# Performance work log

Measured on AMD Instinct MI355X. Metric: run time of the kernel, lower is better.

## Reference

```python
import jax, jax.numpy as jnp
import numpy as np

IMG = 800.0
STRIDES = (4, 8, 16, 32)
SIZES = (32.0, 64.0, 128.0, 256.0)
RATIOS = (0.5, 1.0, 2.0)
A = 3
PRE_NMS_K = 1000
POST_NMS = 512
NMS_TH = 0.7
POOL = 7
_MEAN = np.array([0.485, 0.456, 0.406], np.float32).reshape(3, 1, 1)
_STD = np.array([0.229, 0.224, 0.225], np.float32).reshape(3, 1, 1)


def _conv(x, w, stride=1):
    # x: [C,H,W], w: [O,I,kh,kw]
    return jax.lax.conv_general_dilated(x[None], w, (stride, stride), 'SAME',
                                        dimension_numbers=('NCHW', 'OIHW', 'NCHW'))[0]


def _make_anchors(fh, fw, stride, size):
    cy = (np.arange(fh, dtype=np.float32) + 0.5) * stride
    cx = (np.arange(fw, dtype=np.float32) + 0.5) * stride
    ws = np.array([size / np.sqrt(r) for r in RATIOS], np.float32)
    hs = np.array([size * np.sqrt(r) for r in RATIOS], np.float32)
    gy, gx = np.meshgrid(cy, cx, indexing='ij')
    x1 = gx[..., None] - ws / 2; y1 = gy[..., None] - hs / 2
    x2 = gx[..., None] + ws / 2; y2 = gy[..., None] + hs / 2
    return jnp.asarray(np.stack([x1, y1, x2, y2], -1).reshape(-1, 4))  # [fh*fw*A,4]


def _decode(anchors, deltas):
    aw = anchors[:, 2] - anchors[:, 0]; ah = anchors[:, 3] - anchors[:, 1]
    acx = anchors[:, 0] + aw * 0.5; acy = anchors[:, 1] + ah * 0.5
    dw = jnp.clip(deltas[:, 2], -4.0, 4.0); dh = jnp.clip(deltas[:, 3], -4.0, 4.0)
    cx = acx + deltas[:, 0] * aw; cy = acy + deltas[:, 1] * ah
    w = aw * jnp.exp(dw); h = ah * jnp.exp(dh)
    boxes = jnp.stack([cx - w * 0.5, cy - h * 0.5, cx + w * 0.5, cy + h * 0.5], -1)
    return jnp.clip(boxes, 0.0, IMG)


def _nms(boxes, scores, iou_th, max_out):
    # Greedy NMS with fixed output size (jit-compatible).
    x1, y1, x2, y2 = boxes[:, 0], boxes[:, 1], boxes[:, 2], boxes[:, 3]
    areas = (x2 - x1) * (y2 - y1)

    def body(i, state):
        s, keep = state
        idx = jnp.argmax(s)
        keep = keep.at[i].set(idx)
        ix1 = jnp.maximum(x1, x1[idx]); iy1 = jnp.maximum(y1, y1[idx])
        ix2 = jnp.minimum(x2, x2[idx]); iy2 = jnp.minimum(y2, y2[idx])
        inter = jnp.maximum(ix2 - ix1, 0.0) * jnp.maximum(iy2 - iy1, 0.0)
        iou = inter / (areas + areas[idx] - inter + 1e-6)
        return jnp.where(iou > iou_th, -jnp.inf, s), keep

    _, keep = jax.lax.fori_loop(0, max_out, body, (scores, jnp.zeros(max_out, jnp.int32)))
    return keep


def _roi_align(feat, rois, scale):
    # feat: [C,H,W]; rois: [N,4] in image coords; bilinear, 1 sample per bin.
    C, H, W = feat.shape
    n = rois.shape[0]
    x1 = rois[:, 0] * scale; y1 = rois[:, 1] * scale
    bw = (rois[:, 2] - rois[:, 0]) * scale / POOL
    bh = (rois[:, 3] - rois[:, 1]) * scale / POOL
    j = jnp.arange(POOL, dtype=feat.dtype) + 0.5
    gx = jnp.broadcast_to((x1[:, None] + j * bw[:, None] - 0.5)[:, None, :], (n, POOL, POOL))
    gy = jnp.broadcast_to((y1[:, None] + j * bh[:, None] - 0.5)[:, :, None], (n, POOL, POOL))
    fx = jnp.clip(jnp.floor(gx), 0.0, W - 1); fy = jnp.clip(jnp.floor(gy), 0.0, H - 1)
    x0 = fx.astype(jnp.int32); y0 = fy.astype(jnp.int32)
    x1i = jnp.minimum(x0 + 1, W - 1); y1i = jnp.minimum(y0 + 1, H - 1)
    wx = jnp.clip(gx - fx, 0.0, 1.0); wy = jnp.clip(gy - fy, 0.0, 1.0)
    v = (feat[:, y0, x0] * (1 - wy) * (1 - wx) + feat[:, y0, x1i] * (1 - wy) * wx
         + feat[:, y1i, x0] * wy * (1 - wx) + feat[:, y1i, x1i] * wy * wx)  # [C,N,P,P]
    return jnp.transpose(v, (1, 0, 2, 3))  # [N,C,P,P]


def _forward(x, stem_w, c2_w, c3_w, c4_w, c5_w, fpn2_w, fpn3_w, fpn4_w, fpn5_w,
             rpn_w, rpn_cls_w, rpn_box_w, fc1_w, fc1_b, fc2_w, fc2_b,
             cls_w, cls_b, breg_w, breg_b):
    x = (x - _MEAN) / _STD  # ImageNet normalize
    h = jax.nn.relu(_conv(x, stem_w, 2))      # [64,400,400]
    c2 = jax.nn.relu(_conv(h, c2_w, 2))       # [256,200,200] stride 4
    c3 = jax.nn.relu(_conv(c2, c3_w, 2))      # stride 8
    c4 = jax.nn.relu(_conv(c3, c4_w, 2))      # stride 16
    c5 = jax.nn.relu(_conv(c4, c5_w, 2))      # stride 32
    feats = [_conv(c2, fpn2_w), _conv(c3, fpn3_w), _conv(c4, fpn4_w), _conv(c5, fpn5_w)]

    boxes_l, scores_l = [], []
    for lvl, f in enumerate(feats):
        t = jax.nn.relu(_conv(f, rpn_w))
        fh, fw = f.shape[1], f.shape[2]
        logits = jnp.transpose(_conv(t, rpn_cls_w), (1, 2, 0)).reshape(-1)  # [fh*fw*A]
        deltas = jnp.transpose(_conv(t, rpn_box_w).reshape(A, 4, fh, fw), (2, 3, 0, 1)).reshape(-1, 4)
        anchors = _make_anchors(fh, fw, STRIDES[lvl], SIZES[lvl])
        dec = _decode(anchors, deltas)
        k = min(PRE_NMS_K, logits.shape[0])
        sc, idx = jax.lax.top_k(logits, k)
        boxes_l.append(dec[idx]); scores_l.append(sc)

    boxes = jnp.concatenate(boxes_l, 0)
    scores = jnp.concatenate(scores_l, 0)
    keep = _nms(boxes, scores, NMS_TH, POST_NMS)
    props = boxes[keep]  # [POST_NMS,4]

    pooled = _roi_align(feats[0], props, 1.0 / STRIDES[0])  # [N,256,7,7]
    v = pooled.reshape(POST_NMS, -1)
    v = jax.nn.relu(v @ fc1_w + fc1_b)
    v = jax.nn.relu(v @ fc2_w + fc2_b)
    return v @ cls_w + cls_b, v @ breg_w + breg_b, props, scores[keep]


def setup_inputs() -> dict:
    key = jax.random.key(0)
    ks = jax.random.split(key, 18)

    def he(k, shape):
        fan_in = int(np.prod(shape[1:])) if len(shape) == 4 else shape[0]
        return jax.random.normal(k, shape, jnp.float32) * float(np.sqrt(2.0 / fan_in))

    inp = {'x': jax.random.uniform(ks[0], (3, 800, 800), jnp.float32)}
    inp['stem_w'] = he(ks[1], (64, 3, 7, 7))
    inp['c2_w'] = he(ks[2], (256, 64, 3, 3))
    for i, name in enumerate(['c3_w', 'c4_w', 'c5_w', 'fpn2_w', 'fpn3_w', 'fpn4_w', 'fpn5_w', 'rpn_w']):
        inp[name] = he(ks[3 + i], (256, 256, 3, 3))
    inp['rpn_cls_w'] = he(ks[11], (3, 256, 1, 1))
    inp['rpn_box_w'] = he(ks[12], (12, 256, 1, 1))
    inp['fc1_w'] = he(ks[13], (12544, 1024)); inp['fc1_b'] = jnp.zeros((1024,), jnp.float32)
    inp['fc2_w'] = he(ks[14], (1024, 1024)); inp['fc2_b'] = jnp.zeros((1024,), jnp.float32)
    inp['cls_w'] = he(ks[15], (1024, 2)); inp['cls_b'] = jnp.zeros((2,), jnp.float32)
    inp['breg_w'] = he(ks[16], (1024, 8)); inp['breg_b'] = jnp.zeros((8,), jnp.float32)
    return inp


def reference(x, stem_w, c2_w, c3_w, c4_w, c5_w, fpn2_w, fpn3_w, fpn4_w, fpn5_w,
              rpn_w, rpn_cls_w, rpn_box_w, fc1_w, fc1_b, fc2_w, fc2_b,
              cls_w, cls_b, breg_w, breg_b):
    return _forward(x, stem_w, c2_w, c3_w, c4_w, c5_w, fpn2_w, fpn3_w, fpn4_w, fpn5_w,
                    rpn_w, rpn_cls_w, rpn_box_w, fc1_w, fc1_b, fc2_w, fc2_b,
                    cls_w, cls_b, breg_w, breg_b)
```

## Files before the change

kernel.cpp:

```cpp
#include <hip/hip_runtime.h>
#include <math.h>


#define DI __device__ __forceinline__

typedef short short8 __attribute__((ext_vector_type(8)));
typedef float float16v __attribute__((ext_vector_type(16)));

DI unsigned fkey(float f) {
  unsigned u = __float_as_uint(f);
  return (u & 0x80000000u) ? ~u : (u | 0x80000000u);
}

DI unsigned short f2bf(float f) {
  unsigned u = __float_as_uint(f);
  unsigned r = (u + 0x7FFFu + ((u >> 16) & 1u)) >> 16;
  return (unsigned short)r;
}

DI void rp256(const float* src, float* dst, int j) {
  int co = j & 15; int r = j >> 4; int kk = r % 9; int r2 = r / 9;
  int ci = r2 & 255; int z = r2 >> 8;
  dst[j] = src[((size_t)(z * 16 + co) * 256 + ci) * 9 + kk];
}

__global__ void repack_all(
    const float* __restrict__ wf2, const float* __restrict__ wf3,
    const float* __restrict__ wrpn, const float* __restrict__ wc2,
    const float* __restrict__ wc3, const float* __restrict__ wc4,
    const float* __restrict__ wc5, const float* __restrict__ wf4,
    const float* __restrict__ wf5, const float* __restrict__ wstem,
    float* __restrict__ wpkA, float* __restrict__ wpkB,
    float* __restrict__ wpkC, float* __restrict__ wpkD,
    float* __restrict__ wpkE, float* __restrict__ wpkF,
    float* __restrict__ wpkG, float* __restrict__ wpkH,
    float* __restrict__ wpkI, float* __restrict__ wpkS) {
  const int SZ = 589824, SZD = 147456;
  const int D0 = 3 * SZ;
  const int D1 = D0 + SZD;
  const int D2 = D1 + 5 * SZ;
  const int D3 = D2 + 9408;
  int i = blockIdx.x * 256 + threadIdx.x;
  if (i >= D3) return;
  if (i < D0) {
    const float* src = (i < SZ) ? wf2 : (i < 2 * SZ) ? wf3 : wrpn;
    float* dst = (i < SZ) ? wpkA : (i < 2 * SZ) ? wpkB : wpkC;
    rp256(src, dst, i % SZ);
  } else if (i < D1) {
    int j = i - D0;
    int co = j & 15; int r = j >> 4; int kk = r % 9; int r2 = r / 9;
    int ci = r2 & 63; int z = r2 >> 6;
    wpkD[j] = wc2[((size_t)(z * 16 + co) * 64 + ci) * 9 + kk];
  } else if (i < D2) {
    int j = i - D1;
    int seg = j / SZ; j -= seg * SZ;
    const float* src = (seg == 0) ? wc3 : (seg == 1) ? wc4
                       : (seg == 2) ? wc5 : (seg == 3) ? wf4 : wf5;
    float* dst = (seg == 0) ? wpkE : (seg == 1) ? wpkF
                 : (seg == 2) ? wpkG : (seg == 3) ? wpkH : wpkI;
    rp256(src, dst, j);
  } else {
    int j = i - D2;
    int co = j & 3; int r = j >> 2;
    int k = r % 147; int z = r / 147;
    wpkS[j] = wstem[(size_t)(z * 4 + co) * 147 + k];
  }
}

__global__ __launch_bounds__(256) void stem_conv(const float* __restrict__ x,
                                                 const float* __restrict__ wpkS,
                                                 float* __restrict__ out) {
  __shared__ float tin[3 * 37 * 37];
  const int x0 = blockIdx.x * 16, y0 = blockIdx.y * 16, co0 = blockIdx.z * 4;
  const int tid = threadIdx.x;
  const int ix0 = x0 * 2 - 2, iy0 = y0 * 2 - 2;
  const float mean[3] = {0.485f, 0.456f, 0.406f};
  const float stdv[3] = {0.229f, 0.224f, 0.225f};
  for (int i = tid; i < 3 * 37 * 37; i += 256) {
    int c = i / 1369, r = i % 1369, yy = r / 37, xx = r % 37;
    int gy = iy0 + yy, gx = ix0 + xx;
    float v = 0.f;
    if ((unsigned)gy < 800u && (unsigned)gx < 800u)
      v = __fdiv_rn(__fsub_rn(x[c * 640000 + gy * 800 + gx], mean[c]), stdv[c]);
    tin[i] = v;
  }
  __syncthreads();
  const int tx = tid & 15, ty = tid >> 4;
  float acc[4] = {0.f, 0.f, 0.f, 0.f};
  const float4* wq = (const float4*)(wpkS + (size_t)blockIdx.z * 588);
  for (int c = 0; c < 3; ++c)
    for (int ky = 0; ky < 7; ++ky)
#pragma unroll
      for (int kx = 0; kx < 7; ++kx) {
        float v = tin[c * 1369 + (ty * 2 + ky) * 37 + (tx * 2 + kx)];
        float4 wv = wq[c * 49 + ky * 7 + kx];
        acc[0] = fmaf(v, wv.x, acc[0]);
        acc[1] = fmaf(v, wv.y, acc[1]);
        acc[2] = fmaf(v, wv.z, acc[2]);
        acc[3] = fmaf(v, wv.w, acc[3]);
      }
  int ox = x0 + tx, oy = y0 + ty;
#pragma unroll
  for (int co = 0; co < 4; ++co)
    out[(size_t)(co0 + co) * 160000 + oy * 400 + ox] = fmaxf(acc[co], 0.f);
}

template <int CHUNK, bool RELU, bool TT>
DI void conv32_body(const float* __restrict__ in,
                    const float* __restrict__ wpk, float* __restrict__ out,
                    int Cin, int Hin, int Win, int Hout, int Wout, int bx,
                    int by, int bz,
                    float (*tin2)[((CHUNK * 612 + 255) / 256) * 256]) {
  constexpr int TILE = CHUNK * 612;
  constexpr int NS = (TILE + 255) / 256;
  const int tid = threadIdx.x;
  const int tx = tid & 15, ty = tid >> 4;
  const int x0 = bx * 32, y0 = by * 16;
  const int ix0 = x0 - 1, iy0 = y0 - 1;
  const size_t HWin = (size_t)Hin * Win;

  int goff[NS];
#pragma unroll
  for (int j = 0; j < NS; ++j) {
    int e = j * 256 + tid;
    int c = e / 612, r = e % 612;
    int yy = r / 34, xx = r % 34;
    int gy = iy0 + yy, gx = ix0 + xx;
    bool ok = (e < TILE) && ((unsigned)gy < (unsigned)Hin) &&
              ((unsigned)gx < (unsigned)Win);
    goff[j] = ok ? (int)((size_t)c * HWin + (size_t)gy * Win + gx) : -1;
  }

  float acc0[16], acc1[16];
#pragma unroll
  for (int co = 0; co < 16; ++co) { acc0[co] = 0.f; acc1[co] = 0.f; }

  float stg[NS];
#pragma unroll
  for (int j = 0; j < NS; ++j)
    stg[j] = (goff[j] >= 0) ? in[goff[j]] : 0.f;
#pragma unroll
  for (int j = 0; j < NS; ++j) tin2[0][j * 256 + tid] = stg[j];
  __syncthreads();

  int buf = 0;
  for (int cb = 0; cb < Cin; cb += CHUNK) {
    const bool more = (cb + CHUNK) < Cin;
    if (more) {
      const float* gsrc = in + (size_t)(cb + CHUNK) * HWin;
#pragma unroll
      for (int j = 0; j < NS; ++j)
        stg[j] = (goff[j] >= 0) ? gsrc[goff[j]] : 0.f;
    }
    for (int ci = 0; ci < CHUNK; ++ci) {
      const float4* wq = (const float4*)(wpk +
          ((size_t)bz * Cin + (size_t)(cb + ci)) * 144);
#pragma unroll
      for (int ky = 0; ky < 3; ++ky) {
        const float* tb = &tin2[buf][ci * 612 + (ty + ky) * 34 + 2 * tx];
        float2 d0 = *(const float2*)tb;
        float2 d1 = *(const float2*)(tb + 2);
#pragma unroll
        for (int kx = 0; kx < 3; ++kx) {
          float v0 = (kx == 0) ? d0.x : (kx == 1) ? d0.y : d1.x;
          float v1 = (kx == 0) ? d0.y : (kx == 1) ? d1.x : d1.y;
          const int kk = ky * 3 + kx;
          float4 w0 = wq[kk * 4 + 0];
          float4 w1 = wq[kk * 4 + 1];
          float4 w2 = wq[kk * 4 + 2];
          float4 w3 = wq[kk * 4 + 3];
          acc0[0]  = fmaf(v0, w0.x, acc0[0]);
          acc0[1]  = fmaf(v0, w0.y, acc0[1]);
          acc0[2]  = fmaf(v0, w0.z, acc0[2]);
          acc0[3]  = fmaf(v0, w0.w, acc0[3]);
          acc1[0]  = fmaf(v1, w0.x, acc1[0]);
          acc1[1]  = fmaf(v1, w0.y, acc1[1]);
          acc1[2]  = fmaf(v1, w0.z, acc1[2]);
          acc1[3]  = fmaf(v1, w0.w, acc1[3]);
          acc0[4]  = fmaf(v0, w1.x, acc0[4]);
          acc0[5]  = fmaf(v0, w1.y, acc0[5]);
          acc0[6]  = fmaf(v0, w1.z, acc0[6]);
          acc0[7]  = fmaf(v0, w1.w, acc0[7]);
          acc1[4]  = fmaf(v1, w1.x, acc1[4]);
          acc1[5]  = fmaf(v1, w1.y, acc1[5]);
          acc1[6]  = fmaf(v1, w1.z, acc1[6]);
          acc1[7]  = fmaf(v1, w1.w, acc1[7]);
          acc0[8]  = fmaf(v0, w2.x, acc0[8]);
          acc0[9]  = fmaf(v0, w2.y, acc0[9]);
          acc0[10] = fmaf(v0, w2.z, acc0[10]);
          acc0[11] = fmaf(v0, w2.w, acc0[11]);
          acc1[8]  = fmaf(v1, w2.x, acc1[8]);
          acc1[9]  = fmaf(v1, w2.y, acc1[9]);
          acc1[10] = fmaf(v1, w2.z, acc1[10]);
          acc1[11] = fmaf(v1, w2.w, acc1[11]);
          acc0[12] = fmaf(v0, w3.x, acc0[12]);
          acc0[13] = fmaf(v0, w3.y, acc0[13]);
          acc0[14] = fmaf(v0, w3.z, acc0[14]);
          acc0[15] = fmaf(v0, w3.w, acc0[15]);
          acc1[12] = fmaf(v1, w3.x, acc1[12]);
          acc1[13] = fmaf(v1, w3.y, acc1[13]);
          acc1[14] = fmaf(v1, w3.z, acc1[14]);
          acc1[15] = fmaf(v1, w3.w, acc1[15]);
        }
      }
    }
    if (more) {
#pragma unroll
      for (int j = 0; j < NS; ++j) tin2[buf ^ 1][j * 256 + tid] = stg[j];
    }
    __syncthreads();
    buf ^= 1;
  }

  const int co0 = bz * 16;
  int oy = y0 + ty;
  if (oy < Hout) {
    int ox = x0 + 2 * tx;
    if (TT) {
      if (ox < Wout) {
        float* o = out + (size_t)(oy * Wout + ox) * 256 + co0;
#pragma unroll
        for (int co = 0; co < 16; ++co) {
          float a = acc0[co];
          if (RELU) a = fmaxf(a, 0.f);
          o[co] = a;
        }
      }
      if (ox + 1 < Wout) {
        float* o = out + (size_t)(oy * Wout + ox + 1) * 256 + co0;
#pragma unroll
        for (int co = 0; co < 16; ++co) {
          float a = acc1[co];
          if (RELU) a = fmaxf(a, 0.f);
          o[co] = a;
        }
      }
    } else {
      if (ox + 1 < Wout) {
#pragma unroll
        for (int co = 0; co < 16; ++co) {
          float a = acc0[co], b = acc1[co];
          if (RELU) { a = fmaxf(a, 0.f); b = fmaxf(b, 0.f); }
          float2 st; st.x = a; st.y = b;
          *(float2*)&out[(size_t)(co0 + co) * Hout * Wout +
                         (size_t)oy * Wout + ox] = st;
        }
      } else if (ox < Wout) {
#pragma unroll
        for (int co = 0; co < 16; ++co) {
          float a = acc0[co];
          if (RELU) a = fmaxf(a, 0.f);
          out[(size_t)(co0 + co) * Hout * Wout + (size_t)oy * Wout + ox] = a;
        }
      }
    }
  }
// ... 310 lines not shown
    float dh = fminf(fmaxf(a[3 + an * 4 + 3], -4.f), 4.f);
    float cx = __fadd_rn(acx, __fmul_rn(dx, aw));
    float cy = __fadd_rn(acy, __fmul_rn(dy, ah));
    float w_ = __fmul_rn(aw, expf(dw));
    float h_ = __fmul_rn(ah, expf(dh));
    int idx = p * 3 + an;
    float* bo = boxes4 + boff;
    bo[idx * 4 + 0] =
        fminf(fmaxf(__fsub_rn(cx, __fmul_rn(w_, 0.5f)), 0.f), 800.f);
    bo[idx * 4 + 1] =
        fminf(fmaxf(__fsub_rn(cy, __fmul_rn(h_, 0.5f)), 0.f), 800.f);
    bo[idx * 4 + 2] =
        fminf(fmaxf(__fadd_rn(cx, __fmul_rn(w_, 0.5f)), 0.f), 800.f);
    bo[idx * 4 + 3] =
        fminf(fmaxf(__fadd_rn(cy, __fmul_rn(h_, 0.5f)), 0.f), 800.f);
    scores4[soff + idx] = a[an];
    atomicAdd(&hist4[lvl * 65536 + (fkey(a[an]) >> 16)], 1);
  }
}

__global__ __launch_bounds__(256) void scan_hi_all(int* __restrict__ hist4,
                                                   int* __restrict__ sel4) {
  __shared__ int csum[256];
  int* hist = hist4 + blockIdx.x * 65536;
  int* sel = sel4 + blockIdx.x * 8;
  const int k = 1000;
  int t = threadIdx.x;
  int s = 0;
  for (int i = 0; i < 256; ++i) s += hist[t * 256 + i];
  csum[t] = s;
  __syncthreads();
  if (t == 0) {
    int cum = 0;
    bool done = false;
    for (int c = 255; c >= 0; --c) {
      if (cum + csum[c] >= k) {
        int cc = cum;
        for (int b = c * 256 + 255;; --b) {
          int h = hist[b];
          if (cc + h >= k) {
            sel[0] = b; sel[1] = k - cc; sel[2] = cc;
            done = true;
            break;
          }
          cc += h;
        }
        break;
      }
      cum += csum[c];
    }
    if (!done) { sel[0] = 0; sel[1] = k - cum; sel[2] = cum; }
  }
  __syncthreads();
  int4 z4; z4.x = 0; z4.y = 0; z4.z = 0; z4.w = 0;
  for (int i = t; i < 16384; i += 256) ((int4*)hist)[i] = z4;
}

DI void lvl_seg(int b, int& lvl, int& base, int& N, int& soff, int& boff) {
  if (b < 469) { lvl = 0; base = 0; N = 120000; soff = 0; boff = 0; }
  else if (b < 587) { lvl = 1; base = 469; N = 30000; soff = 120000;
                      boff = 480000; }
  else if (b < 617) { lvl = 2; base = 587; N = 7500; soff = 150000;
                      boff = 600000; }
  else { lvl = 3; base = 617; N = 1875; soff = 157500; boff = 630000; }
}

__global__ void hist_lo_all(const float* __restrict__ scores4,
                            const int* __restrict__ sel4,
                            int* __restrict__ hist4) {
  int lvl, base, N, soff, boff;
  lvl_seg(blockIdx.x, lvl, base, N, soff, boff);
  int i = (blockIdx.x - base) * 256 + threadIdx.x;
  if (i >= N) return;
  unsigned bsel = (unsigned)sel4[lvl * 8 + 0];
  unsigned key = fkey(scores4[soff + i]);
  if ((key >> 16) == bsel)
    atomicAdd(&hist4[lvl * 65536 + (key & 0xffffu)], 1);
}

__global__ __launch_bounds__(256) void scan_lo_all(
    const int* __restrict__ hist4, int* __restrict__ sel4) {
  __shared__ int csum[256];
  const int* hist = hist4 + blockIdx.x * 65536;
  int* sel = sel4 + blockIdx.x * 8;
  int t = threadIdx.x;
  int s = 0;
  for (int i = 0; i < 256; ++i) s += hist[t * 256 + i];
  csum[t] = s;
  __syncthreads();
  if (t == 0) {
    int r = sel[1], b = sel[0], cc_hi = sel[2];
    int cum = 0;
    bool done = false;
    for (int c = 255; c >= 0; --c) {
      if (cum + csum[c] >= r) {
        int cc = cum;
        for (int l = c * 256 + 255;; --l) {
          int h = hist[l];
          if (cc + h >= r) {
            sel[3] = (int)(((unsigned)b << 16) | (unsigned)l);
            sel[4] = cc_hi + cc;
            sel[5] = r - cc;
            sel[6] = 0;
            sel[7] = 0;
            done = true;
            break;
          }
          cc += h;
        }
        break;
      }
      cum += csum[c];
    }
    if (!done) {
      sel[3] = (int)((unsigned)b << 16);
      sel[4] = cc_hi; sel[5] = r; sel[6] = 0; sel[7] = 0;
    }
  }
}

__global__ void compact_all(const float* __restrict__ scores4,
                            const float* __restrict__ boxes4,
                            int* __restrict__ sel4,
                            float* __restrict__ out_s,
                            float* __restrict__ out_b) {
  int lvl, base, N, soff, boff;
  lvl_seg(blockIdx.x, lvl, base, N, soff, boff);
  int i = (blockIdx.x - base) * 256 + threadIdx.x;
  if (i >= N) return;
  int* sel = sel4 + lvl * 8;
  unsigned key = fkey(scores4[soff + i]);
  unsigned kth = (unsigned)sel[3];
  int pos = -1;
  if (key > kth) {
    pos = atomicAdd(&sel[6], 1);
  } else if (key == kth) {
    int e = atomicAdd(&sel[7], 1);
    if (e < sel[5]) pos = sel[4] + e;
  }
  if (pos >= 0) {
    int o = lvl * 1000 + pos;
    out_s[o] = scores4[soff + i];
    const float* bo = boxes4 + boff;
    out_b[o * 4 + 0] = bo[i * 4 + 0];
    out_b[o * 4 + 1] = bo[i * 4 + 1];
    out_b[o * 4 + 2] = bo[i * 4 + 2];
    out_b[o * 4 + 3] = bo[i * 4 + 3];
  }
}

#define NMS_N 4000
#define NMS_W 63

__global__ __launch_bounds__(256) void rank_kernel(const float* __restrict__ s,
                                                   int* __restrict__ order) {
  __shared__ float ls[NMS_N];
  for (int i = threadIdx.x; i < NMS_N; i += 256) ls[i] = s[i];
  __syncthreads();
  int i = blockIdx.x * 256 + threadIdx.x;
  if (i >= NMS_N) return;
  float si = ls[i];
  int cnt = 0;
  for (int j = 0; j < NMS_N; ++j) {
    float sj = ls[j];
    cnt += (sj > si) || (sj == si && j < i);
  }
  order[cnt] = i;
}

__global__ __launch_bounds__(256) void supp_kernel(
    const float* __restrict__ boxes, unsigned long long* __restrict__ supp) {
  __shared__ float sx1[NMS_W * 64], sy1[NMS_W * 64];
  __shared__ float sx2[NMS_W * 64], sy2[NMS_W * 64];
  for (int i = threadIdx.x; i < NMS_W * 64; i += 256) {
    float x1 = 0.f, y1 = 0.f, x2 = 0.f, y2 = 0.f;
    if (i < NMS_N) {
      x1 = boxes[i * 4 + 0]; y1 = boxes[i * 4 + 1];
      x2 = boxes[i * 4 + 2]; y2 = boxes[i * 4 + 3];
    }
    sx1[i] = x1; sy1[i] = y1; sx2[i] = x2; sy2[i] = y2;
  }
  __syncthreads();
  const int wave = threadIdx.x >> 6, lane = threadIdx.x & 63;
  for (int rr = 0; rr < 16; ++rr) {
    int i = blockIdx.x * 16 + rr;
    if (i >= NMS_N) return;
    float ix1 = sx1[i], iy1 = sy1[i], ix2 = sx2[i], iy2 = sy2[i];
    float ia = __fmul_rn(__fsub_rn(ix2, ix1), __fsub_rn(iy2, iy1));
    for (int w = wave; w < NMS_W; w += 4) {
      int j = w * 64 + lane;
      float jx1 = sx1[j], jy1 = sy1[j], jx2 = sx2[j], jy2 = sy2[j];
      float ja = __fmul_rn(__fsub_rn(jx2, jx1), __fsub_rn(jy2, jy1));
      float cx1 = fmaxf(jx1, ix1), cy1 = fmaxf(jy1, iy1);
      float cx2 = fminf(jx2, ix2), cy2 = fminf(jy2, iy2);
      float iw = fmaxf(__fsub_rn(cx2, cx1), 0.f);
      float ih = fmaxf(__fsub_rn(cy2, cy1), 0.f);
      float inter = __fmul_rn(iw, ih);
      float denom = __fadd_rn(__fsub_rn(__fadd_rn(ja, ia), inter), 1e-6f);
      bool pred = __fdiv_rn(inter, denom) > 0.7f;
      unsigned long long bits = __ballot(pred);
      if (lane == 0) supp[(size_t)i * NMS_W + w] = bits;
    }
  }
}

__global__ __launch_bounds__(64) void nms_scan(
    const unsigned long long* __restrict__ supp, const int* __restrict__ order,
    const float* __restrict__ boxes, const float* __restrict__ scores,
    float* __restrict__ props, float* __restrict__ out_props,
    float* __restrict__ out_scores) {
  __shared__ unsigned long long removed[NMS_W];
  __shared__ int keepL[512];
  const int tid = threadIdx.x;
  if (tid < NMS_W) removed[tid] = 0ull;
  __syncthreads();
  int kept = 0, sticky = -1;
  for (int g = 0; g < NMS_W && sticky < 0 && kept < 512; ++g) {
    int pos = g * 64 + tid;
    int c = (pos < NMS_N) ? order[pos] : -1;
    while (kept < 512) {
      bool avail = (c >= 0) && !((removed[c >> 6] >> (c & 63)) & 1ull);
      unsigned long long bal = __ballot(avail);
      if (bal == 0ull) break;
      int fl = __ffsll((unsigned long long)bal) - 1;
      int ck = __shfl(c, fl);
      if (tid == 0) keepL[kept] = ck;
      kept++;
      unsigned long long w =
          (tid < NMS_W) ? supp[(size_t)ck * NMS_W + tid] : 0ull;
      unsigned long long selfw = __shfl(w, ck >> 6);
      if (tid < NMS_W) removed[tid] |= w;
      __syncthreads();
      if (!((selfw >> (ck & 63)) & 1ull)) { sticky = ck; break; }
    }
  }
  __syncthreads();
  const int fill = (sticky >= 0) ? sticky : 0;
  for (int k = tid; k < 512; k += 64) {
    int idx = (k < kept) ? keepL[k] : fill;
    float x1 = boxes[idx * 4 + 0], y1 = boxes[idx * 4 + 1];
    float x2 = boxes[idx * 4 + 2], y2 = boxes[idx * 4 + 3];
    props[k * 4 + 0] = x1; props[k * 4 + 1] = y1;
    props[k * 4 + 2] = x2; props[k * 4 + 3] = y2;
    out_props[k * 4 + 0] = x1; out_props[k * 4 + 1] = y1;
    out_props[k * 4 + 2] = x2; out_props[k * 4 + 3] = y2;
    out_scores[k] = scores[idx];
  }
}

__global__ __launch_bounds__(256) void roi_align_kernel(
    const float* __restrict__ feat, const float* __restrict__ rois,
    float* __restrict__ out) {
  __shared__ int sx0[7], sx1i[7], sy0[7], sy1i[7];
  __shared__ float swx[7], swy[7];
  const int n = blockIdx.x;
  if (threadIdx.x < 14) {
    int i = threadIdx.x % 7;
    bool isY = threadIdx.x >= 7;
    float r0 = rois[n * 4 + (isY ? 1 : 0)];
    float r1 = rois[n * 4 + (isY ? 3 : 2)];
    float a = __fmul_rn(r0, 0.25f);
    float b = __fdiv_rn(__fmul_rn(__fsub_rn(r1, r0), 0.25f), 7.0f);
    float g = __fsub_rn(__fadd_rn(a, __fmul_rn((float)i + 0.5f, b)), 0.5f);
    float fl = fminf(fmaxf(floorf(g), 0.f), 199.f);
    int i0 = (int)fl;
    int i1 = min(i0 + 1, 199);
    float wf = fminf(fmaxf(__fsub_rn(g, fl), 0.f), 1.f);
    if (isY) { sy0[i] = i0; sy1i[i] = i1; swy[i] = wf; }
    else     { sx0[i] = i0; sx1i[i] = i1; swx[i] = wf; }
  }
  __syncthreads();
  const int c = threadIdx.x;
  const float* fc_ = feat + (size_t)c * 40000;
  float* o = out + (size_t)n * 12544 + c * 49;
  for (int s = 0; s < 49; ++s) {
    int py = s / 7, px = s % 7;
    int y0 = sy0[py], y1 = sy1i[py], x0 = sx0[px], x1 = sx1i[px];
    float wy = swy[py], wx = swx[px];
    float v00 = fc_[y0 * 200 + x0], v01 = fc_[y0 * 200 + x1];
    float v10 = fc_[y1 * 200 + x0], v11 = fc_[y1 * 200 + x1];
    float v = ((v00 * (1.f - wy)) * (1.f - wx)) + ((v01 * (1.f - wy)) * wx) +
              ((v10 * wy) * (1.f - wx)) + ((v11 * wy) * wx);
    o[s] = v;
  }
}

__global__ void cast_a(const float* __restrict__ in,
                       unsigned short* __restrict__ out, int n) {
  int i = blockIdx.x * 256 + threadIdx.x;
  if (i < n) out[i] = f2bf(in[i]);
}

__global__ __launch_bounds__(256) void cast_bt(const float* __restrict__ B,
                                               unsigned short* __restrict__ Bt,
                                               int K, int N) {
  __shared__ float tile[32][33];
  const int k0 = blockIdx.y * 32, n0 = blockIdx.x * 32;
  const int tx = threadIdx.x & 31, ty = threadIdx.x >> 5;
  for (int r = ty; r < 32; r += 8)
    tile[r][tx] = B[(size_t)(k0 + r) * N + n0 + tx];
  __syncthreads();
  for (int r = ty; r < 32; r += 8)
    Bt[(size_t)(n0 + r) * K + k0 + tx] = f2bf(tile[tx][r]);
}

__global__ __launch_bounds__(256) void fc_mfma(
    const unsigned short* __restrict__ A,
    const unsigned short* __restrict__ Bt,
    float* __restrict__ Cp, int M, int N, int K, int kLen) {
  const int tid = threadIdx.x;
  const int lane = tid & 63, wave = tid >> 6;
  const int n = lane & 31, half = lane >> 5;
  const int bm = blockIdx.y * 128 + wave * 32;
  const int bn = blockIdx.x * 64;
  const int k0s = blockIdx.z * kLen;
  const unsigned short* arow = A + (size_t)(bm + n) * K + half * 8;
  const unsigned short* b0row = Bt + (size_t)(bn + n) * K + half * 8;
  const unsigned short* b1row = Bt + (size_t)(bn + 32 + n) * K + half * 8;
  float16v acc0, acc1;
#pragma unroll
  for (int r = 0; r < 16; ++r) { acc0[r] = 0.f; acc1[r] = 0.f; }
  for (int k0 = k0s; k0 < k0s + kLen; k0 += 16) {
    short8 a = *(const short8*)(arow + k0);
    short8 b0 = *(const short8*)(b0row + k0);
    short8 b1 = *(const short8*)(b1row + k0);
    acc0 = __builtin_amdgcn_mfma_f32_32x32x16_bf16(a, b0, acc0, 0, 0, 0);
    acc1 = __builtin_amdgcn_mfma_f32_32x32x16_bf16(a, b1, acc1, 0, 0, 0);
  }
  float* Cz = Cp + (size_t)blockIdx.z * M * N;
#pragma unroll
  for (int r = 0; r < 16; ++r) {
    int row = bm + (r & 3) + 8 * (r >> 2) + 4 * half;
    Cz[(size_t)row * N + bn + n] = acc0[r];
    Cz[(size_t)row * N + bn + 32 + n] = acc1[r];
  }
}

__global__ void fc_combine(const float* __restrict__ p,
                           const float* __restrict__ bias,
                           float* __restrict__ out, int MN, int N, int S) {
  int i = blockIdx.x * 256 + threadIdx.x;
  if (i >= MN) return;
  float v = 0.f;
  for (int s = 0; s < S; ++s) v += p[(size_t)s * MN + i];
  out[i] = fmaxf(v + bias[i % N], 0.f);
}

__global__ __launch_bounds__(64) void heads_kernel(
    const float* __restrict__ v, const float* __restrict__ wc,
    const float* __restrict__ bc, const float* __restrict__ wb,
    const float* __restrict__ bbias, float* __restrict__ out) {
  const int m = blockIdx.x;
  const int lane = threadIdx.x;
  float acc[10];
#pragma unroll
  for (int o = 0; o < 10; ++o) acc[o] = 0.f;
  for (int k = lane; k < 1024; k += 64) {
    float x = v[(size_t)m * 1024 + k];
    acc[0] = fmaf(x, wc[k * 2 + 0], acc[0]);
    acc[1] = fmaf(x, wc[k * 2 + 1], acc[1]);
#pragma unroll
    for (int o = 0; o < 8; ++o) acc[2 + o] = fmaf(x, wb[k * 8 + o], acc[2 + o]);
  }
#pragma unroll
  for (int off = 32; off > 0; off >>= 1)
#pragma unroll
    for (int o = 0; o < 10; ++o) acc[o] += __shfl_down(acc[o], off);
  if (lane == 0) {
    out[m * 2 + 0] = acc[0] + bc[0];
    out[m * 2 + 1] = acc[1] + bc[1];
#pragma unroll
    for (int o = 0; o < 8; ++o) out[1024 + m * 8 + o] = acc[2 + o] + bbias[o];
  }
}

extern "C" void kernel_launch(void* const* d_in, const int* in_sizes, int n_in,
                              void* d_out, int out_size, void* d_ws,
                              size_t ws_size, hipStream_t stream) {
  const float* x      = (const float*)d_in[0];
  const float* w_stem = (const float*)d_in[1];
  const float* w_c2   = (const float*)d_in[2];
  const float* w_c3   = (const float*)d_in[3];
  const float* w_c4   = (const float*)d_in[4];
  const float* w_c5   = (const float*)d_in[5];
  const float* w_f2   = (const float*)d_in[6];
  const float* w_f3   = (const float*)d_in[7];
  const float* w_f4   = (const float*)d_in[8];
  const float* w_f5   = (const float*)d_in[9];
  const float* w_rpn  = (const float*)d_in[10];
  const float* w_cls  = (const float*)d_in[11];
  const float* w_box  = (const float*)d_in[12];
  const float* w_fc1  = (const float*)d_in[13];
  const float* b_fc1  = (const float*)d_in[14];
  const float* w_fc2  = (const float*)d_in[15];
  const float* b_fc2  = (const float*)d_in[16];
  const float* w_clsh = (const float*)d_in[17];
  const float* b_clsh = (const float*)d_in[18];
  const float* w_breg = (const float*)d_in[19];
  const float* b_breg = (const float*)d_in[20];
  float* dout = (float*)d_out;

  float* ws = (float*)d_ws;
  float* stem = ws;
  float* c2   = stem + 10240000;
  float* c3   = c2 + 10240000;
  float* c4   = c3 + 2560000;
  float* c5   = c4 + 640000;
  float* f2   = c5 + 160000;
  float* f3   = f2 + 10240000;
  float* f4   = f3 + 2560000;
  float* f5   = f4 + 640000;
  float* boxes_all  = f5 + 160000;
  float* scores_all = boxes_all + 16000;
  float* props      = scores_all + 4000;
  int*   histOld = (int*)(props + 2048);
  int*   sel  = histOld + 65536;
  float* wpkA = (float*)(sel + 16);
  float* wpkB = wpkA + 589824;
  float* wpkC = wpkB + 589824;
  float* wpkD = wpkC + 589824;
  float* wpkE = wpkD + 147456;
  float* wpkF = wpkE + 589824;
  float* wpkG = wpkF + 589824;
  float* wpkH = wpkG + 589824;
  float* wpkI = wpkH + 589824;
  float* wpkS = wpkI + 589824;
  float* tt0 = stem;
  float* tt1 = c3;
  float* tt2 = wpkF;
  float* tt3 = wpkH;
  int*   hist4 = (int*)wpkE;
  int*   sel4  = histOld;
  float* boxes4  = c4;
  float* scores4 = c5;
  int*   order  = (int*)c3;
  unsigned long long* supp =
      (unsigned long long*)(c3 + 8192);
  float* pooled = stem;
  float* fc1o   = stem + 6422528;
  float* fc2o   = fc1o + 524288;
  float* fcp    = fc2o + 524288;
  unsigned short* Abf1 = (unsigned short*)c2;
  unsigned short* Bt1  = (unsigned short*)(c2 + 3211264);
  unsigned short* Abf2 = (unsigned short*)c3;
  unsigned short* Bt2  = (unsigned short*)(c3 + 262144);

  repack_all<<<19045, 256, 0, stream>>>(
      w_f2, w_f3, w_rpn, w_c2, w_c3, w_c4, w_c5, w_f4, w_f5, w_stem,
      wpkA, wpkB, wpkC, wpkD, wpkE, wpkF, wpkG, wpkH, wpkI, wpkS);

  stem_conv<<<dim3(25, 25, 16), 256, 0, stream>>>(x, wpkS, stem);
  conv16_s2<4, true><<<dim3(13, 13, 16), 256, 0, stream>>>(
      stem, wpkD, c2, 64, 400, 400, 200, 200);
  conv16_s2<4, true><<<dim3(7, 7, 16), 256, 0, stream>>>(
      c2, wpkE, c3, 256, 200, 200, 100, 100);
  conv16_s2<4, true><<<dim3(4, 4, 16), 256, 0, stream>>>(
      c3, wpkF, c4, 256, 100, 100, 50, 50);
  conv16_s2<4, true><<<dim3(2, 2, 16), 256, 0, stream>>>(
      c4, wpkG, c5, 256, 50, 50, 25, 25);
  conv32_lat<4, false, false><<<1904, 256, 0, stream>>>(
      c2, wpkA, f2, 256, 200, 200, 7, 13, 1456,
      c3, wpkB, f3, 256, 100, 100, 4, 7);
  conv16_lat<8, false, false><<<320, 256, 0, stream>>>(
      c4, wpkH, f4, 256, 50, 50, 4, 4, 256,
      c5, wpkI, f5, 256, 25, 25, 2, 2);

  conv32_lat<4, true, true><<<1904, 256, 0, stream>>>(
      f2, wpkC, tt0, 256, 200, 200, 7, 13, 1456,
      f3, wpkC, tt1, 256, 100, 100, 4, 7);
  conv16_lat<8, true, true><<<320, 256, 0, stream>>>(
      f4, wpkC, tt2, 256, 50, 50, 4, 4, 256,
      f5, wpkC, tt3, 256, 25, 25, 2, 2);

  hipMemsetAsync(hist4, 0, 4 * 65536 * sizeof(int), stream);
  rpn_decode_all<<<210, 256, 0, stream>>>(tt0, tt1, tt2, tt3, w_cls, w_box,
                                          boxes4, scores4, hist4);
  scan_hi_all<<<4, 256, 0, stream>>>(hist4, sel4);
  hist_lo_all<<<625, 256, 0, stream>>>(scores4, sel4, hist4);
  scan_lo_all<<<4, 256, 0, stream>>>(hist4, sel4);
  compact_all<<<625, 256, 0, stream>>>(scores4, boxes4, sel4, scores_all,
                                       boxes_all);

  rank_kernel<<<16, 256, 0, stream>>>(scores_all, order);
  supp_kernel<<<250, 256, 0, stream>>>(boxes_all, supp);
  nms_scan<<<1, 64, 0, stream>>>(supp, order, boxes_all, scores_all, props,
                                 dout + 5120, dout + 7168);

  roi_align_kernel<<<512, 256, 0, stream>>>(f2, props, pooled);
  cast_a<<<(6422528 + 255) / 256, 256, 0, stream>>>(pooled, Abf1, 6422528);
  cast_bt<<<dim3(32, 392), 256, 0, stream>>>(w_fc1, Bt1, 12544, 1024);
  fc_mfma<<<dim3(16, 4, 4), 256, 0, stream>>>(Abf1, Bt1, fcp, 512, 1024, 12544,
                                              3136);
  fc_combine<<<2048, 256, 0, stream>>>(fcp, b_fc1, fc1o, 524288, 1024, 4);
  cast_a<<<(524288 + 255) / 256, 256, 0, stream>>>(fc1o, Abf2, 524288);
  cast_bt<<<dim3(32, 32), 256, 0, stream>>>(w_fc2, Bt2, 1024, 1024);
  fc_mfma<<<dim3(16, 4, 4), 256, 0, stream>>>(Abf2, Bt2, fcp, 512, 1024, 1024,
                                              256);
  fc_combine<<<2048, 256, 0, stream>>>(fcp, b_fc2, fc2o, 524288, 1024, 4);
  heads_kernel<<<512, 64, 0, stream>>>(fc2o, w_clsh, b_clsh, w_breg, b_breg,
                                       dout);
}
```

Before: 4.406 ms.

## Fuse bf16 casts into producers, merge NMS and weight-cast launches, widen stem

The stem conv now computes 8 output channels per block instead of 4, with the weight repack changed to match, so each shared-memory input value feeds more FMAs. ROI-align and the fc1 combine now write bf16 directly, which removes the separate cast_a passes and their fp32 intermediates. The rank and suppression-matrix kernels are merged into one launch that branches on block index, and both fc weight transposes are merged into one cast kernel. Together these cut kernel launches and memory traffic, at the cost of more registers in the stem conv and a larger shared buffer in the merged NMS kernel.

```diff
diff --git a/kernel.cpp b/kernel.cpp
--- a/kernel.cpp
+++ b/kernel.cpp
@@ -61,9 +61,9 @@
     rp256(src, dst, j);
   } else {
     int j = i - D2;
-    int co = j & 3; int r = j >> 2;
-    int k = r % 147; int z = r / 147;
-    wpkS[j] = wstem[(size_t)(z * 4 + co) * 147 + k];
+    int co = j & 7; int t = j >> 3;
+    int k = t % 147; int z = t / 147;
+    wpkS[j] = wstem[(size_t)(z * 8 + co) * 147 + k];
   }
 }
 
@@ -71,7 +71,7 @@
                                                  const float* __restrict__ wpkS,
                                                  float* __restrict__ out) {
   __shared__ float tin[3 * 37 * 37];
-  const int x0 = blockIdx.x * 16, y0 = blockIdx.y * 16, co0 = blockIdx.z * 4;
+  const int x0 = blockIdx.x * 16, y0 = blockIdx.y * 16, co0 = blockIdx.z * 8;
   const int tid = threadIdx.x;
   const int ix0 = x0 * 2 - 2, iy0 = y0 * 2 - 2;
   const float mean[3] = {0.485f, 0.456f, 0.406f};
@@ -86,22 +86,30 @@
   }
   __syncthreads();
   const int tx = tid & 15, ty = tid >> 4;
-  float acc[4] = {0.f, 0.f, 0.f, 0.f};
-  const float4* wq = (const float4*)(wpkS + (size_t)blockIdx.z * 588);
+  float acc[8];
+#pragma unroll
+  for (int co = 0; co < 8; ++co) acc[co] = 0.f;
+  const float4* wq = (const float4*)(wpkS + (size_t)blockIdx.z * 1176);
   for (int c = 0; c < 3; ++c)
     for (int ky = 0; ky < 7; ++ky)
 #pragma unroll
       for (int kx = 0; kx < 7; ++kx) {
         float v = tin[c * 1369 + (ty * 2 + ky) * 37 + (tx * 2 + kx)];
-        float4 wv = wq[c * 49 + ky * 7 + kx];
-        acc[0] = fmaf(v, wv.x, acc[0]);
-        acc[1] = fmaf(v, wv.y, acc[1]);
-        acc[2] = fmaf(v, wv.z, acc[2]);
-        acc[3] = fmaf(v, wv.w, acc[3]);
+        int k = c * 49 + ky * 7 + kx;
+        float4 w0 = wq[k * 2 + 0];
+        float4 w1 = wq[k * 2 + 1];
+        acc[0] = fmaf(v, w0.x, acc[0]);
+        acc[1] = fmaf(v, w0.y, acc[1]);
+        acc[2] = fmaf(v, w0.z, acc[2]);
+        acc[3] = fmaf(v, w0.w, acc[3]);
+        acc[4] = fmaf(v, w1.x, acc[4]);
+        acc[5] = fmaf(v, w1.y, acc[5]);
+        acc[6] = fmaf(v, w1.z, acc[6]);
+        acc[7] = fmaf(v, w1.w, acc[7]);
       }
   int ox = x0 + tx, oy = y0 + ty;
 #pragma unroll
-  for (int co = 0; co < 4; ++co)
+  for (int co = 0; co < 8; ++co)
     out[(size_t)(co0 + co) * 160000 + oy * 400 + ox] = fmaxf(acc[co], 0.f);
 }
 
@@ -718,54 +726,58 @@
 #define NMS_N 4000
 #define NMS_W 63
 
-__global__ __launch_bounds__(256) void rank_kernel(const float* __restrict__ s,
-                                                   int* __restrict__ order) {
-  __shared__ float ls[NMS_N];
-  for (int i = threadIdx.x; i < NMS_N; i += 256) ls[i] = s[i];
-  __syncthreads();
-  int i = blockIdx.x * 256 + threadIdx.x;
-  if (i >= NMS_N) return;
-  float si = ls[i];
-  int cnt = 0;
-  for (int j = 0; j < NMS_N; ++j) {
-    float sj = ls[j];
-    cnt += (sj > si) || (sj == si && j < i);
-  }
-  order[cnt] = i;
-}
-
-__global__ __launch_bounds__(256) void supp_kernel(
+__global__ __launch_bounds__(256) void rank_supp(
+    const float* __restrict__ s, int* __restrict__ order,
     const float* __restrict__ boxes, unsigned long long* __restrict__ supp) {
-  __shared__ float sx1[NMS_W * 64], sy1[NMS_W * 64];
-  __shared__ float sx2[NMS_W * 64], sy2[NMS_W * 64];
-  for (int i = threadIdx.x; i < NMS_W * 64; i += 256) {
-    float x1 = 0.f, y1 = 0.f, x2 = 0.f, y2 = 0.f;
-    if (i < NMS_N) {
-      x1 = boxes[i * 4 + 0]; y1 = boxes[i * 4 + 1];
-      x2 = boxes[i * 4 + 2]; y2 = boxes[i * 4 + 3];
-    }
-    sx1[i] = x1; sy1[i] = y1; sx2[i] = x2; sy2[i] = y2;
-  }
-  __syncthreads();
-  const int wave = threadIdx.x >> 6, lane = threadIdx.x & 63;
-  for (int rr = 0; rr < 16; ++rr) {
-    int i = blockIdx.x * 16 + rr;
+  __shared__ float sbuf[NMS_W * 64 * 4];
+  if (blockIdx.x < 16) {
+    float* ls = sbuf;
+    for (int i = threadIdx.x; i < NMS_N; i += 256) ls[i] = s[i];
+    __syncthreads();
+    int i = blockIdx.x * 256 + threadIdx.x;
     if (i >= NMS_N) return;
-    float ix1 = sx1[i], iy1 = sy1[i], ix2 = sx2[i], iy2 = sy2[i];
-    float ia = __fmul_rn(__fsub_rn(ix2, ix1), __fsub_rn(iy2, iy1));
-    for (int w = wave; w < NMS_W; w += 4) {
-      int j = w * 64 + lane;
-      float jx1 = sx1[j], jy1 = sy1[j], jx2 = sx2[j], jy2 = sy2[j];
-      float ja = __fmul_rn(__fsub_rn(jx2, jx1), __fsub_rn(jy2, jy1));
-      float cx1 = fmaxf(jx1, ix1), cy1 = fmaxf(jy1, iy1);
-      float cx2 = fminf(jx2, ix2), cy2 = fminf(jy2, iy2);
-      float iw = fmaxf(__fsub_rn(cx2, cx1), 0.f);
-      float ih = fmaxf(__fsub_rn(cy2, cy1), 0.f);
-      float inter = __fmul_rn(iw, ih);
-      float denom = __fadd_rn(__fsub_rn(__fadd_rn(ja, ia), inter), 1e-6f);
-      bool pred = __fdiv_rn(inter, denom) > 0.7f;
-      unsigned long long bits = __ballot(pred);
-      if (lane == 0) supp[(size_t)i * NMS_W + w] = bits;
+    float si = ls[i];
+    int cnt = 0;
+    for (int j = 0; j < NMS_N; ++j) {
+      float sj = ls[j];
+      cnt += (sj > si) || (sj == si && j < i);
+    }
+    order[cnt] = i;
+  } else {
+    const int bid = blockIdx.x - 16;
+    float* sx1 = sbuf;
+    float* sy1 = sbuf + NMS_W * 64;
+    float* sx2 = sbuf + NMS_W * 64 * 2;
+    float* sy2 = sbuf + NMS_W * 64 * 3;
+    for (int i = threadIdx.x; i < NMS_W * 64; i += 256) {
+      float x1 = 0.f, y1 = 0.f, x2 = 0.f, y2 = 0.f;
+      if (i < NMS_N) {
+        x1 = boxes[i * 4 + 0]; y1 = boxes[i * 4 + 1];
+        x2 = boxes[i * 4 + 2]; y2 = boxes[i * 4 + 3];
+      }
+      sx1[i] = x1; sy1[i] = y1; sx2[i] = x2; sy2[i] = y2;
+    }
+    __syncthreads();
+    const int wave = threadIdx.x >> 6, lane = threadIdx.x & 63;
+    for (int rr = 0; rr < 16; ++rr) {
+      int i = bid * 16 + rr;
+      if (i >= NMS_N) return;
+      float ix1 = sx1[i], iy1 = sy1[i], ix2 = sx2[i], iy2 = sy2[i];
+      float ia = __fmul_rn(__fsub_rn(ix2, ix1), __fsub_rn(iy2, iy1));
+      for (int w = wave; w < NMS_W; w += 4) {
+        int j = w * 64 + lane;
+        float jx1 = sx1[j], jy1 = sy1[j], jx2 = sx2[j], jy2 = sy2[j];
+        float ja = __fmul_rn(__fsub_rn(jx2, jx1), __fsub_rn(jy2, jy1));
+        float cx1 = fmaxf(jx1, ix1), cy1 = fmaxf(jy1, iy1);
+        float cx2 = fminf(jx2, ix2), cy2 = fminf(jy2, iy2);
+        float iw = fmaxf(__fsub_rn(cx2, cx1), 0.f);
+        float ih = fmaxf(__fsub_rn(cy2, cy1), 0.f);
+        float inter = __fmul_rn(iw, ih);
+        float denom = __fadd_rn(__fsub_rn(__fadd_rn(ja, ia), inter), 1e-6f);
+        bool pred = __fdiv_rn(inter, denom) > 0.7f;
+        unsigned long long bits = __ballot(pred);
+        if (lane == 0) supp[(size_t)i * NMS_W + w] = bits;
+      }
     }
   }
 }
@@ -816,7 +828,7 @@
 
 __global__ __launch_bounds__(256) void roi_align_kernel(
     const float* __restrict__ feat, const float* __restrict__ rois,
-    float* __restrict__ out) {
+    unsigned short* __restrict__ outBf) {
   __shared__ int sx0[7], sx1i[7], sy0[7], sy1i[7];
   __shared__ float swx[7], swy[7];
   const int n = blockIdx.x;
@@ -838,7 +850,7 @@
   __syncthreads();
   const int c = threadIdx.x;
   const float* fc_ = feat + (size_t)c * 40000;
-  float* o = out + (size_t)n * 12544 + c * 49;
+  unsigned short* o = outBf + (size_t)n * 12544 + c * 49;
   for (int s = 0; s < 49; ++s) {
     int py = s / 7, px = s % 7;
     int y0 = sy0[py], y1 = sy1i[py], x0 = sx0[px], x1 = sx1i[px];
@@ -847,22 +859,25 @@
     float v10 = fc_[y1 * 200 + x0], v11 = fc_[y1 * 200 + x1];
     float v = ((v00 * (1.f - wy)) * (1.f - wx)) + ((v01 * (1.f - wy)) * wx) +
               ((v10 * wy) * (1.f - wx)) + ((v11 * wy) * wx);
-    o[s] = v;
-  }
-}
-
-__global__ void cast_a(const float* __restrict__ in,
-                       unsigned short* __restrict__ out, int n) {
-  int i = blockIdx.x * 256 + threadIdx.x;
-  if (i < n) out[i] = f2bf(in[i]);
-}
-
-__global__ __launch_bounds__(256) void cast_bt(const float* __restrict__ B,
-                                               unsigned short* __restrict__ Bt,
-                                               int K, int N) {
+    o[s] = f2bf(v);
+  }
+}
+
+__global__ __launch_bounds__(256) void cast_bt_all(
+    const float* __restrict__ B1, unsigned short* __restrict__ Bt1,
+    const float* __restrict__ B2, unsigned short* __restrict__ Bt2) {
   __shared__ float tile[32][33];
-  const int k0 = blockIdx.y * 32, n0 = blockIdx.x * 32;
   const int tx = threadIdx.x & 31, ty = threadIdx.x >> 5;
+  int bid = blockIdx.x;
+  const float* B; unsigned short* Bt; int K, N, k0, n0;
+  if (bid < 12544) {
+    B = B1; Bt = Bt1; K = 12544; N = 1024;
+    n0 = (bid & 31) * 32; k0 = (bid >> 5) * 32;
+  } else {
+    bid -= 12544;
+    B = B2; Bt = Bt2; K = 1024; N = 1024;
+    n0 = (bid & 31) * 32; k0 = (bid >> 5) * 32;
+  }
   for (int r = ty; r < 32; r += 8)
     tile[r][tx] = B[(size_t)(k0 + r) * N + n0 + tx];
   __syncthreads();
@@ -900,6 +915,17 @@
     Cz[(size_t)row * N + bn + n] = acc0[r];
     Cz[(size_t)row * N + bn + 32 + n] = acc1[r];
   }
+}
+
+__global__ void fc_combine_bf(const float* __restrict__ p,
+                              const float* __restrict__ bias,
+                              unsigned short* __restrict__ outBf, int MN,
+                              int N, int S) {
+  int i = blockIdx.x * 256 + threadIdx.x;
+  if (i >= MN) return;
+  float v = 0.f;
+  for (int s = 0; s < S; ++s) v += p[(size_t)s * MN + i];
+  outBf[i] = f2bf(fmaxf(v + bias[i % N], 0.f));
 }
 
 __global__ void fc_combine(const float* __restrict__ p,
@@ -1002,9 +1028,7 @@
   int*   order  = (int*)c3;
   unsigned long long* supp =
       (unsigned long long*)(c3 + 8192);
-  float* pooled = stem;
-  float* fc1o   = stem + 6422528;
-  float* fc2o   = fc1o + 524288;
+  float* fc2o   = stem + 6422528;
   float* fcp    = fc2o + 524288;
   unsigned short* Abf1 = (unsigned short*)c2;
   unsigned short* Bt1  = (unsigned short*)(c2 + 3211264);
@@ -1015,7 +1039,7 @@
       w_f2, w_f3, w_rpn, w_c2, w_c3, w_c4, w_c5, w_f4, w_f5, w_stem,
       wpkA, wpkB, wpkC, wpkD, wpkE, wpkF, wpkG, wpkH, wpkI, wpkS);
 
-  stem_conv<<<dim3(25, 25, 16), 256, 0, stream>>>(x, wpkS, stem);
+  stem_conv<<<dim3(25, 25, 8), 256, 0, stream>>>(x, wpkS, stem);
   conv16_s2<4, true><<<dim3(13, 13, 16), 256, 0, stream>>>(
       stem, wpkD, c2, 64, 400, 400, 200, 200);
   conv16_s2<4, true><<<dim3(7, 7, 16), 256, 0, stream>>>(
@@ -1047,19 +1071,15 @@
   compact_all<<<625, 256, 0, stream>>>(scores4, boxes4, sel4, scores_all,
                                        boxes_all);
 
-  rank_kernel<<<16, 256, 0, stream>>>(scores_all, order);
-  supp_kernel<<<250, 256, 0, stream>>>(boxes_all, supp);
+  rank_supp<<<266, 256, 0, stream>>>(scores_all, order, boxes_all, supp);
   nms_scan<<<1, 64, 0, stream>>>(supp, order, boxes_all, scores_all, props,
                                  dout + 5120, dout + 7168);
 
-  roi_align_kernel<<<512, 256, 0, stream>>>(f2, props, pooled);
-  cast_a<<<(6422528 + 255) / 256, 256, 0, stream>>>(pooled, Abf1, 6422528);
-  cast_bt<<<dim3(32, 392), 256, 0, stream>>>(w_fc1, Bt1, 12544, 1024);
+  roi_align_kernel<<<512, 256, 0, stream>>>(f2, props, Abf1);
+  cast_bt_all<<<12544 + 1024, 256, 0, stream>>>(w_fc1, Bt1, w_fc2, Bt2);
   fc_mfma<<<dim3(16, 4, 4), 256, 0, stream>>>(Abf1, Bt1, fcp, 512, 1024, 12544,
                                               3136);
-  fc_combine<<<2048, 256, 0, stream>>>(fcp, b_fc1, fc1o, 524288, 1024, 4);
-  cast_a<<<(524288 + 255) / 256, 256, 0, stream>>>(fc1o, Abf2, 524288);
-  cast_bt<<<dim3(32, 32), 256, 0, stream>>>(w_fc2, Bt2, 1024, 1024);
+  fc_combine_bf<<<2048, 256, 0, stream>>>(fcp, b_fc1, Abf2, 524288, 1024, 4);
   fc_mfma<<<dim3(16, 4, 4), 256, 0, stream>>>(Abf2, Bt2, fcp, 512, 1024, 1024,
                                               256);
   fc_combine<<<2048, 256, 0, stream>>>(fcp, b_fc2, fc2o, 524288, 1024, 4);
```

Result: no change. 4.322 ms (-1.9%).
